# Optimization experiments

Measured on AMD Instinct MI355X. Metric: run time of the kernel, lower is better.

## Reference

```python
import jax, jax.numpy as jnp
import numpy as np

B, S, E, H = 4, 2048, 1024, 16
D = E // H  # head_size = 64

def setup_inputs() -> dict:
    key = jax.random.key(0)
    k1, k2, k3 = jax.random.split(key, 3)
    x = jax.random.normal(k1, (B, S, E), dtype=jnp.float32)
    # torch Linear weight is (out,in); we store transposed (in,out) for x @ W
    w_attn = jax.random.normal(k2, (E, 3 * E), dtype=jnp.float32) * (1.0 / np.sqrt(E))
    w_proj = jax.random.normal(k3, (E, E), dtype=jnp.float32) * (1.0 / np.sqrt(E))
    return {"x": x, "w_attn": w_attn, "w_proj": w_proj}

def reference(x, w_attn, w_proj):
    b, s, e = x.shape
    qkv = x @ w_attn                      # (B,S,3E)
    q, k, v = jnp.split(qkv, 3, axis=2)
    # (B,S,H,D) -> (B,H,S,D)
    q = q.reshape(b, s, H, D).transpose(0, 2, 1, 3)
    k = k.reshape(b, s, H, D).transpose(0, 2, 1, 3)
    v = v.reshape(b, s, H, D).transpose(0, 2, 1, 3)
    scale = 1.0 / np.sqrt(D).astype(np.float32)
    att = jnp.einsum('bhqd,bhkd->bhqk', q, k) * scale  # (B,H,S,S)
    causal = jnp.tril(jnp.ones((s, s), dtype=bool))
    att = jnp.where(causal[None, None, :, :], att, jnp.float32(-jnp.inf))
    att = jax.nn.softmax(att, axis=-1)
    # dropout layers are identity in eval mode
    y = jnp.einsum('bhqk,bhkd->bhqd', att, v)          # (B,H,S,D)
    y = y.transpose(0, 2, 1, 3).reshape(b, s, e)       # (B,S,E)
    return y @ w_proj
```

## Files before the change

### kernel.cpp

```cpp
#include <hip/hip_runtime.h>
#include <hip/hip_bf16.h>
#include <cstdint>

typedef __attribute__((ext_vector_type(8))) short bf16x8;
typedef __attribute__((ext_vector_type(4))) short short4v;
typedef __attribute__((ext_vector_type(4))) float f32x4;

#define MFMA(a, b, c) __builtin_amdgcn_mfma_f32_16x16x32_bf16((a), (b), (c), 0, 0, 0)

__device__ __forceinline__ unsigned short f2bf(float f) {
  union { float f; unsigned int u; } v;
  v.f = f;
  unsigned int r = v.u + 0x7FFFu + ((v.u >> 16) & 1u);
  return (unsigned short)(r >> 16);
}

__device__ __forceinline__ unsigned short f2bf_ru(float f) {
  union { float f; unsigned int u; } v;
  v.f = f;
  return (unsigned short)((v.u + 0x8000u) >> 16);
}

__device__ __forceinline__ void async_cp16(const unsigned short* g, unsigned short* l) {
  __builtin_amdgcn_global_load_lds(
      (const __attribute__((address_space(1))) unsigned int*)g,
      (__attribute__((address_space(3))) unsigned int*)l, 16, 0, 0);
}

__global__ __launch_bounds__(256) void cvt_x(const float* __restrict__ in,
                                             unsigned short* __restrict__ out) {
  size_t i = ((size_t)blockIdx.x * 256 + threadIdx.x) * 8;
  float4 a = *(const float4*)(in + i);
  float4 b = *(const float4*)(in + i + 4);
  bf16x8 p;
  p[0] = (short)f2bf(a.x); p[1] = (short)f2bf(a.y);
  p[2] = (short)f2bf(a.z); p[3] = (short)f2bf(a.w);
  p[4] = (short)f2bf(b.x); p[5] = (short)f2bf(b.y);
  p[6] = (short)f2bf(b.z); p[7] = (short)f2bf(b.w);
  *(bf16x8*)(out + i) = p;
}

__global__ __launch_bounds__(256) void transpose_cvt(const float* __restrict__ in,
                                                     unsigned short* __restrict__ out,
                                                     int K, int N) {
  __shared__ float tile[64][65];
  int k0 = blockIdx.x * 64;
  int n0 = blockIdx.y * 64;
  int c = threadIdx.x & 63;
  int rb = threadIdx.x >> 6;
#pragma unroll
  for (int i = 0; i < 16; ++i) {
    int r = rb * 16 + i;
    tile[r][c] = in[(size_t)(k0 + r) * N + (n0 + c)];
  }
  __syncthreads();
#pragma unroll
  for (int i = 0; i < 16; ++i) {
    int r = rb * 16 + i;
    out[(size_t)(n0 + r) * K + (k0 + c)] = f2bf(tile[c][r]);
  }
}

__global__ __launch_bounds__(256) void gemm_qkv(const unsigned short* __restrict__ X,
                                                const unsigned short* __restrict__ WT,
                                                unsigned short* __restrict__ qb,
                                                unsigned short* __restrict__ kb,
                                                unsigned short* __restrict__ vt) {
  const int K = 1024;
  __shared__ unsigned short As[128 * 64];
  __shared__ unsigned short Bs[128 * 64];
  int t = threadIdx.x, lane = t & 63, w = t >> 6;
  int quad = lane >> 4, l15 = lane & 15;
  int sl7 = l15 & 7;
  int wm = (w >> 1) * 64, wn = (w & 1) * 64;
  int row0 = blockIdx.y * 128, col0 = blockIdx.x * 128;
  int srow = w * 8 + (lane >> 3);
  int schunk = (lane & 7) ^ (lane >> 3);
  const unsigned short* aSrc = X + (size_t)(row0 + srow) * K + schunk * 8;
  const unsigned short* bSrc = WT + (size_t)(col0 + srow) * K + schunk * 8;
  unsigned short* ldsA = &As[(w * 8) * 64];
  unsigned short* ldsB = &Bs[(w * 8) * 64];
  f32x4 zero4 = {0.f, 0.f, 0.f, 0.f};
  f32x4 acc[4][4];
#pragma unroll
  for (int i = 0; i < 4; ++i)
#pragma unroll
    for (int j = 0; j < 4; ++j) acc[i][j] = zero4;

  for (int k0 = 0; k0 < K; k0 += 64) {
    __syncthreads();
#pragma unroll
    for (int i = 0; i < 4; ++i)
      async_cp16(aSrc + (size_t)i * 32 * K + k0, ldsA + i * 32 * 64);
#pragma unroll
    for (int i = 0; i < 4; ++i)
      async_cp16(bSrc + (size_t)i * 32 * K + k0, ldsB + i * 32 * 64);
    __syncthreads();
#pragma unroll
    for (int h = 0; h < 2; ++h) {
      bf16x8 af[4], bfr[4];
#pragma unroll
      for (int mt = 0; mt < 4; ++mt)
        af[mt] = *(const bf16x8*)&As[(wm + mt * 16 + l15) * 64 +
                                     ((h * 4 + quad) ^ sl7) * 8];
#pragma unroll
      for (int nt = 0; nt < 4; ++nt)
        bfr[nt] = *(const bf16x8*)&Bs[(wn + nt * 16 + l15) * 64 +
                                      ((h * 4 + quad) ^ sl7) * 8];
#pragma unroll
      for (int mt = 0; mt < 4; ++mt)
#pragma unroll
        for (int nt = 0; nt < 4; ++nt)
          acc[mt][nt] = MFMA(af[mt], bfr[nt], acc[mt][nt]);
    }
  }

  const float qscale = 0.125f * 1.4426950408889634f;
#pragma unroll
  for (int mt = 0; mt < 4; ++mt) {
    int rix0 = row0 + wm + mt * 16 + quad * 4;
    int b = rix0 >> 11;
    int s0 = rix0 & 2047;
#pragma unroll
    for (int nt = 0; nt < 4; ++nt) {
      int c = col0 + wn + nt * 16 + l15;
      int which = c >> 10;
      int e = c & 1023;
      int h = e >> 6, d = e & 63;
      size_t bh = (size_t)b * 16 + h;
      if (which == 2) {
        short4v pv;
#pragma unroll
        for (int r = 0; r < 4; ++r) pv[r] = (short)f2bf(acc[mt][nt][r]);
        *(short4v*)(vt + (bh * 64 + d) * 2048 + s0) = pv;
      } else {
        unsigned short* dst = (which == 0) ? qb : kb;
        float sc = (which == 0) ? qscale : 1.0f;
#pragma unroll
        for (int r = 0; r < 4; ++r)
          dst[(bh * 2048 + (s0 + r)) * 64 + d] = f2bf(acc[mt][nt][r] * sc);
      }
    }
  }
}

__global__ __launch_bounds__(256, 2) void flash_attn(const unsigned short* __restrict__ qb,
                                                     const unsigned short* __restrict__ kb,
                                                     const unsigned short* __restrict__ vt,
                                                     unsigned short* __restrict__ yb) {
  __shared__ unsigned short Ks[2][64 * 64];
  __shared__ unsigned short P[4][16 * 68];
  int idx = blockIdx.x;
  int p = idx >> 6;
  int sub = idx & 63;
  int bh = (sub & 7) * 8 + (sub >> 3);
  int t = threadIdx.x, lane = t & 63, w = t >> 6;
  int quad = lane >> 4, l15 = lane & 15;
  unsigned short* Pw = P[w];
  f32x4 zero4 = {0.f, 0.f, 0.f, 0.f};
  bf16x8 ones;
#pragma unroll
  for (int i = 0; i < 8; ++i) ones[i] = (short)0x3F80;
  int b = bh >> 4, h = bh & 15;

  int srow_st = t >> 3;
  int sslot = (t & 7) ^ (srow_st & 7);
  const unsigned short* kp0 =
      kb + ((size_t)bh * 2048 + srow_st) * 64 + sslot * 8;
  const unsigned short* kp1 = kp0 + 32 * 64;
  const unsigned short* Vb = vt + (size_t)bh * (64 * 2048);
  int rslot0 = (quad ^ (l15 & 7)) * 8;
  int rslot1 = ((quad ^ 4) ^ (l15 & 7)) * 8;

  for (int seg = 0; seg < 2; ++seg) {
    int qt = seg ? p : (15 - p);
    int qrow0 = qt * 128 + w * 32;
    int ktmax = 2 * qt + 1;

    bf16x8 aq0[2], aq1[2];
#pragma unroll
    for (int s = 0; s < 2; ++s) {
      const unsigned short* Qp =
          qb + ((size_t)bh * 2048 + qrow0 + s * 16 + l15) * 64 + quad * 8;
      aq0[s] = *(const bf16x8*)Qp;
      aq1[s] = *(const bf16x8*)(Qp + 32);
    }
    f32x4 o[2][4], accl[2];
#pragma unroll
    for (int s = 0; s < 2; ++s) {
      accl[s] = zero4;
#pragma unroll
      for (int nt = 0; nt < 4; ++nt) o[s][nt] = zero4;
    }

    __syncthreads();
    async_cp16(kp0, &Ks[0][t * 8]);
    async_cp16(kp1, &Ks[0][2048 + t * 8]);
    int cur = 0;

    for (int kt = 0; kt <= ktmax; ++kt) {
      int kbase = kt * 64;
      __syncthreads();
      if (kt < ktmax) {
        const unsigned short* nk = kp0 + (size_t)(kbase + 64) * 64;
        async_cp16(nk, &Ks[cur ^ 1][t * 8]);
        async_cp16(nk + 32 * 64, &Ks[cur ^ 1][2048 + t * 8]);
      }
      if (kbase <= qrow0 + 31) {
        const unsigned short* Kc = &Ks[cur][0];
        bf16x8 vf0[4], vf1[4];
#pragma unroll
        for (int nt = 0; nt < 4; ++nt) {
          const unsigned short* Vp =
              Vb + (size_t)(nt * 16 + l15) * 2048 + kbase + quad * 8;
          vf0[nt] = *(const bf16x8*)Vp;
          vf1[nt] = *(const bf16x8*)(Vp + 32);
        }
        bf16x8 kf0[4], kf1[4];
#pragma unroll
        for (int nt = 0; nt < 4; ++nt) {
          kf0[nt] = *(const bf16x8*)&Kc[(nt * 16 + l15) * 64 + rslot0];
          kf1[nt] = *(const bf16x8*)&Kc[(nt * 16 + l15) * 64 + rslot1];
        }

#pragma unroll
        for (int s = 0; s < 2; ++s) {
          int rowb = qrow0 + s * 16;
          if (kbase <= rowb + 15) {
            f32x4 sv[4];
#pragma unroll
            for (int nt = 0; nt < 4; ++nt) {
              f32x4 z = zero4;
              z = MFMA(aq0[s], kf0[nt], z);
              z = MFMA(aq1[s], kf1[nt], z);
              sv[nt] = z;
            }
            if (kbase + 63 > rowb) {
#pragma unroll
              for (int nt = 0; nt < 4; ++nt) {
                int col = kbase + nt * 16 + l15;
#pragma unroll
                for (int r = 0; r < 4; ++r)
                  if (col > rowb + quad * 4 + r) sv[nt][r] = -1e30f;
              }
            }
#pragma unroll
            for (int nt = 0; nt < 4; ++nt)
#pragma unroll
              for (int r = 0; r < 4; ++r) {
                float pv = __builtin_amdgcn_exp2f(sv[nt][r]);
                Pw[(quad * 4 + r) * 68 + nt * 16 + l15] = f2bf_ru(pv);
              }
            bf16x8 ap0 = *(const bf16x8*)&Pw[l15 * 68 + quad * 8];
            bf16x8 ap1 = *(const bf16x8*)&Pw[l15 * 68 + 32 + quad * 8];
            accl[s] = MFMA(ap0, ones, accl[s]);
            accl[s] = MFMA(ap1, ones, accl[s]);
#pragma unroll
            for (int nt = 0; nt < 4; ++nt) {
              o[s][nt] = MFMA(ap0, vf0[nt], o[s][nt]);
              o[s][nt] = MFMA(ap1, vf1[nt], o[s][nt]);
            }
          }
        }
      }
      cur ^= 1;
    }

#pragma unroll
    for (int s = 0; s < 2; ++s) {
      float inv[4];
#pragma unroll
      for (int r = 0; r < 4; ++r) inv[r] = 1.0f / accl[s][r];
#pragma unroll
      for (int nt = 0; nt < 4; ++nt) {
        int e = h * 64 + nt * 16 + l15;
#pragma unroll
        for (int r = 0; r < 4; ++r) {
          int srow_g = qrow0 + s * 16 + quad * 4 + r;
          yb[((size_t)b * 2048 + srow_g) * 1024 + e] = f2bf(o[s][nt][r] * inv[r]);
        }
      }
    }
  }
}

__global__ __launch_bounds__(256) void gemm_proj(const unsigned short* __restrict__ Y,
                                                 const unsigned short* __restrict__ WT,
                                                 float* __restrict__ out) {
  const int K = 1024;
  __shared__ unsigned short As[128 * 64];
  __shared__ unsigned short Bs[128 * 64];
  int t = threadIdx.x, lane = t & 63, w = t >> 6;
  int quad = lane >> 4, l15 = lane & 15;
  int sl7 = l15 & 7;
  int wm = (w >> 1) * 64, wn = (w & 1) * 64;
  int row0 = blockIdx.y * 128, col0 = blockIdx.x * 128;
  int srow = w * 8 + (lane >> 3);
  int schunk = (lane & 7) ^ (lane >> 3);
  const unsigned short* aSrc = Y + (size_t)(row0 + srow) * K + schunk * 8;
  const unsigned short* bSrc = WT + (size_t)(col0 + srow) * K + schunk * 8;
  unsigned short* ldsA = &As[(w * 8) * 64];
  unsigned short* ldsB = &Bs[(w * 8) * 64];
  f32x4 zero4 = {0.f, 0.f, 0.f, 0.f};
  f32x4 acc[4][4];
#pragma unroll
  for (int i = 0; i < 4; ++i)
#pragma unroll
    for (int j = 0; j < 4; ++j) acc[i][j] = zero4;

  for (int k0 = 0; k0 < K; k0 += 64) {
    __syncthreads();
#pragma unroll
    for (int i = 0; i < 4; ++i)
      async_cp16(aSrc + (size_t)i * 32 * K + k0, ldsA + i * 32 * 64);
#pragma unroll
    for (int i = 0; i < 4; ++i)
      async_cp16(bSrc + (size_t)i * 32 * K + k0, ldsB + i * 32 * 64);
    __syncthreads();
#pragma unroll
    for (int h = 0; h < 2; ++h) {
      bf16x8 af[4], bfr[4];
#pragma unroll
      for (int mt = 0; mt < 4; ++mt)
        af[mt] = *(const bf16x8*)&As[(wm + mt * 16 + l15) * 64 +
                                     ((h * 4 + quad) ^ sl7) * 8];
#pragma unroll
      for (int nt = 0; nt < 4; ++nt)
        bfr[nt] = *(const bf16x8*)&Bs[(wn + nt * 16 + l15) * 64 +
                                      ((h * 4 + quad) ^ sl7) * 8];
#pragma unroll
      for (int mt = 0; mt < 4; ++mt)
#pragma unroll
        for (int nt = 0; nt < 4; ++nt)
          acc[mt][nt] = MFMA(af[mt], bfr[nt], acc[mt][nt]);
    }
  }

#pragma unroll
  for (int mt = 0; mt < 4; ++mt) {
    int rix0 = row0 + wm + mt * 16 + quad * 4;
#pragma unroll
    for (int nt = 0; nt < 4; ++nt) {
      int c = col0 + wn + nt * 16 + l15;
#pragma unroll
      for (int r = 0; r < 4; ++r)
        out[(size_t)(rix0 + r) * 1024 + c] = acc[mt][nt][r];
    }
  }
}

extern "C" void kernel_launch(void* const* d_in, const int* in_sizes, int n_in,
                              void* d_out, int out_size, void* d_ws, size_t ws_size,
                              hipStream_t stream) {
  const float* x = (const float*)d_in[0];
  const float* w_attn = (const float*)d_in[1];
  const float* w_proj = (const float*)d_in[2];
  float* out = (float*)d_out;
  char* ws = (char*)d_ws;
  unsigned short* wT  = (unsigned short*)(ws + 0);
  unsigned short* wpT = (unsigned short*)(ws + 6291456);
  unsigned short* qb  = (unsigned short*)(ws + 8388608);
  unsigned short* kb  = (unsigned short*)(ws + 25165824);
  unsigned short* vt  = (unsigned short*)(ws + 41943040);
  unsigned short* xyb = (unsigned short*)(ws + 58720256);

  cvt_x<<<4096, 256, 0, stream>>>(x, xyb);
  transpose_cvt<<<dim3(16, 48), 256, 0, stream>>>(w_attn, wT, 1024, 3072);
  transpose_cvt<<<dim3(16, 16), 256, 0, stream>>>(w_proj, wpT, 1024, 1024);
  gemm_qkv<<<dim3(24, 64), 256, 0, stream>>>(xyb, wT, qb, kb, vt);
  flash_attn<<<dim3(512), 256, 0, stream>>>(qb, kb, vt, xyb);
  gemm_proj<<<dim3(8, 64), 256, 0, stream>>>(xyb, wpT, out);
}
```

Baseline: 261.2 us.

## Compute transposed QK^T and keep P in registers instead of LDS round-trip

Swaps the MFMA operands so the score tile comes out transposed. A permuted K-row mapping makes each lane's accumulator values line up with the A-operand layout for the PV MFMA. P is then packed straight into bf16 registers with v_cvt_pk_bf16_f32, which removes the per-wave LDS write/read of P and its shared buffer. The K shared-memory swizzle is changed to match the new row access pattern, and the P rounding changes from round-half-up to the hardware round-to-nearest-even.

```diff
diff --git a/kernel.cpp b/kernel.cpp
--- a/kernel.cpp
+++ b/kernel.cpp
@@ -15,10 +15,10 @@
   return (unsigned short)(r >> 16);
 }
 
-__device__ __forceinline__ unsigned short f2bf_ru(float f) {
-  union { float f; unsigned int u; } v;
-  v.f = f;
-  return (unsigned short)((v.u + 0x8000u) >> 16);
+__device__ __forceinline__ unsigned int cvtpk(float lo, float hi) {
+  unsigned int r;
+  asm("v_cvt_pk_bf16_f32 %0, %1, %2" : "=v"(r) : "v"(lo), "v"(hi));
+  return r;
 }
 
 __device__ __forceinline__ void async_cp16(const unsigned short* g, unsigned short* l) {
@@ -149,14 +149,12 @@
                                                      const unsigned short* __restrict__ vt,
                                                      unsigned short* __restrict__ yb) {
   __shared__ unsigned short Ks[2][64 * 64];
-  __shared__ unsigned short P[4][16 * 68];
   int idx = blockIdx.x;
   int p = idx >> 6;
   int sub = idx & 63;
   int bh = (sub & 7) * 8 + (sub >> 3);
   int t = threadIdx.x, lane = t & 63, w = t >> 6;
   int quad = lane >> 4, l15 = lane & 15;
-  unsigned short* Pw = P[w];
   f32x4 zero4 = {0.f, 0.f, 0.f, 0.f};
   bf16x8 ones;
 #pragma unroll
@@ -164,11 +162,13 @@
   int b = bh >> 4, h = bh & 15;
 
   int srow_st = t >> 3;
-  int sslot = (t & 7) ^ (srow_st & 7);
+  int swz_st = (srow_st & 3) | (((srow_st >> 3) & 1) << 2);
+  int sslot = (t & 7) ^ swz_st;
   const unsigned short* kp0 =
       kb + ((size_t)bh * 2048 + srow_st) * 64 + sslot * 8;
   const unsigned short* kp1 = kp0 + 32 * 64;
   const unsigned short* Vb = vt + (size_t)bh * (64 * 2048);
+  int fbase = (l15 >> 2) * 8 + (l15 & 3);
   int rslot0 = (quad ^ (l15 & 7)) * 8;
   int rslot1 = ((quad ^ 4) ^ (l15 & 7)) * 8;
 
@@ -219,40 +219,48 @@
         bf16x8 kf0[4], kf1[4];
 #pragma unroll
         for (int nt = 0; nt < 4; ++nt) {
-          kf0[nt] = *(const bf16x8*)&Kc[(nt * 16 + l15) * 64 + rslot0];
-          kf1[nt] = *(const bf16x8*)&Kc[(nt * 16 + l15) * 64 + rslot1];
+          int row = fbase + (nt & 1) * 4 + (nt >> 1) * 32;
+          kf0[nt] = *(const bf16x8*)&Kc[row * 64 + rslot0];
+          kf1[nt] = *(const bf16x8*)&Kc[row * 64 + rslot1];
         }
 
 #pragma unroll
         for (int s = 0; s < 2; ++s) {
           int rowb = qrow0 + s * 16;
           if (kbase <= rowb + 15) {
-            f32x4 sv[4];
+            f32x4 pv4[4];
 #pragma unroll
             for (int nt = 0; nt < 4; ++nt) {
               f32x4 z = zero4;
-              z = MFMA(aq0[s], kf0[nt], z);
-              z = MFMA(aq1[s], kf1[nt], z);
-              sv[nt] = z;
+              z = MFMA(kf0[nt], aq0[s], z);
+              z = MFMA(kf1[nt], aq1[s], z);
+              pv4[nt] = z;
             }
             if (kbase + 63 > rowb) {
+              int qg = rowb + l15;
 #pragma unroll
               for (int nt = 0; nt < 4; ++nt) {
-                int col = kbase + nt * 16 + l15;
+                int colb = kbase + quad * 8 + (nt & 1) * 4 + ((nt >> 1) << 5);
 #pragma unroll
                 for (int r = 0; r < 4; ++r)
-                  if (col > rowb + quad * 4 + r) sv[nt][r] = -1e30f;
+                  if (colb + r > qg) pv4[nt][r] = -1e30f;
               }
             }
 #pragma unroll
             for (int nt = 0; nt < 4; ++nt)
 #pragma unroll
-              for (int r = 0; r < 4; ++r) {
-                float pv = __builtin_amdgcn_exp2f(sv[nt][r]);
-                Pw[(quad * 4 + r) * 68 + nt * 16 + l15] = f2bf_ru(pv);
-              }
-            bf16x8 ap0 = *(const bf16x8*)&Pw[l15 * 68 + quad * 8];
-            bf16x8 ap1 = *(const bf16x8*)&Pw[l15 * 68 + 32 + quad * 8];
+              for (int r = 0; r < 4; ++r)
+                pv4[nt][r] = __builtin_amdgcn_exp2f(pv4[nt][r]);
+            union { unsigned int u[4]; bf16x8 v; } A0, A1;
+            A0.u[0] = cvtpk(pv4[0][0], pv4[0][1]);
+            A0.u[1] = cvtpk(pv4[0][2], pv4[0][3]);
+            A0.u[2] = cvtpk(pv4[1][0], pv4[1][1]);
+            A0.u[3] = cvtpk(pv4[1][2], pv4[1][3]);
+            A1.u[0] = cvtpk(pv4[2][0], pv4[2][1]);
+            A1.u[1] = cvtpk(pv4[2][2], pv4[2][3]);
+            A1.u[2] = cvtpk(pv4[3][0], pv4[3][1]);
+            A1.u[3] = cvtpk(pv4[3][2], pv4[3][3]);
+            bf16x8 ap0 = A0.v, ap1 = A1.v;
             accl[s] = MFMA(ap0, ones, accl[s]);
             accl[s] = MFMA(ap1, ones, accl[s]);
 #pragma unroll
```

Measured after the change: 254.9 us. 1.02x faster.
